# Kernel tuning notes

Hardware: AMD Instinct MI355X
Metric: run time of the kernel (lower is better)

The kernel has to match this reference:

```python
import jax, jax.numpy as jnp
import numpy as np

E, D, H, B = 8, 64, 512, 32768  # n_experts, state_dim, hidden width, batch
IN = D + 3  # x, t, sin(omega*t), cos(omega*t)


def setup_inputs() -> dict:
    key = jax.random.key(0)
    ks = jax.random.split(key, 12)
    s = 0.02
    return {
        "t": jax.random.uniform(ks[0], (1,), dtype=jnp.float32),
        "x": jax.random.normal(ks[1], (B, D), dtype=jnp.float32),
        "expert_weights": jax.random.uniform(ks[2], (B, E), dtype=jnp.float32),
        "omega": jnp.arange(1, E + 1, dtype=jnp.float32),  # omega_i = i+1
        "W1": jax.random.normal(ks[3], (E, H, IN), dtype=jnp.float32) * s,
        "b1": jnp.zeros((E, H), dtype=jnp.float32),
        "W2": jax.random.normal(ks[4], (E, H, H), dtype=jnp.float32) * s,
        "b2": jnp.zeros((E, H), dtype=jnp.float32),
        "W3": jax.random.normal(ks[5], (E, H, H), dtype=jnp.float32) * s,
        "b3": jnp.zeros((E, H), dtype=jnp.float32),
        "W4": jax.random.normal(ks[6], (E, D, H), dtype=jnp.float32) * s,
        "b4": jnp.zeros((E, D), dtype=jnp.float32),
    }


def reference(t, x, expert_weights, omega, W1, b1, W2, b2, W3, b3, W4, b4):
    # Dense path of ExpertODEEnsemble.forward: all experts active.
    nB = x.shape[0]
    tb = jnp.broadcast_to(t, (nB,))                       # (B,)
    wt = omega[:, None] * tb[None, :]                     # (E, B)
    # Per-expert inputs: [x, t, sin(wt), cos(wt)] -> (E, B, D+3)
    xe = jnp.broadcast_to(x[None], (E, nB, D))
    te = jnp.broadcast_to(tb[None, :, None], (E, nB, 1))
    inp = jnp.concatenate([xe, te, jnp.sin(wt)[..., None], jnp.cos(wt)[..., None]], axis=-1)
    h = jnp.tanh(jnp.einsum('ebi,ehi->ebh', inp, W1) + b1[:, None, :])
    h = jnp.tanh(jnp.einsum('ebh,egh->ebg', h, W2) + b2[:, None, :])
    h = jnp.tanh(jnp.einsum('ebh,egh->ebg', h, W3) + b3[:, None, :])
    dyn = jnp.einsum('ebh,edh->ebd', h, W4) + b4[:, None, :]   # (E, B, D)
    # Weighted combine: sum_e w[b,e] * dyn[e,b,:]
    dx_dt = jnp.einsum('be,ebd->bd', expert_weights, dyn)
    return dx_dt
```

## Files before the change

### kernel.cpp

```cpp
#include <hip/hip_runtime.h>
#include <hip/hip_bf16.h>


typedef unsigned short ushort_t;
typedef unsigned int u32;
typedef unsigned long long u64;
typedef __attribute__((ext_vector_type(8))) short short8;
typedef __attribute__((ext_vector_type(4))) float floatx4;
typedef __attribute__((ext_vector_type(16))) float floatx16;
typedef __attribute__((ext_vector_type(4))) int intx4;

#define W1A_OFF 0u
#define W2A_OFF 524288u
#define W3A_OFF 4718592u
#define W4A_OFF 8912896u
#define XB_OFF  9437184u
#define B1E_OFF 13631488u

#define SLOTB 16384
#define X_OFF_L 131072
#define SYNC_OFF 147456
#define SMEM_SZ 147552

static __device__ __forceinline__ u32 pk2bf(float a, float b) {
  union { __hip_bfloat162 h; u32 u; } v;
  v.h = __float22bfloat162_rn(make_float2(a, b));
  return v.u;
}

static __device__ __forceinline__ float pade_tanh(float x) {
  float x2 = x * x;
  float num = __builtin_fmaf(x2, __builtin_fmaf(x2, 1.0f, 105.0f), 945.0f);
  float den = __builtin_fmaf(x2, __builtin_fmaf(x2, 15.0f, 420.0f), 945.0f);
  return x * num * __builtin_amdgcn_rcpf(den);
}

static __device__ __forceinline__ void ald16(const void* g, void* l) {
  __builtin_amdgcn_global_load_lds((__attribute__((address_space(1))) void*)g,
                                   (__attribute__((address_space(3))) void*)l,
                                   16, 0, 0);
}

static __device__ __forceinline__ floatx16 mfma32(short8 a, short8 b, floatx16 c) {
  return __builtin_amdgcn_mfma_f32_32x32x16_bf16(a, b, c, 0, 0, 0);
}

static __device__ __forceinline__ int slot8(int g, int b) {
  return ((g + b) & 7) * SLOTB;
}

static __device__ __forceinline__ void waitge(const int* p, int tgt) {
  while (*(volatile const int*)p < tgt) __builtin_amdgcn_s_sleep(1);
  __asm__ __volatile__("" ::: "memory");
}

static __device__ __forceinline__ void waitge4(const int* p, int tgt) {
  for (;;) {
    __asm__ __volatile__("" ::: "memory");
    intx4 v = *(const intx4*)p;
    if (v[0] >= tgt && v[1] >= tgt && v[2] >= tgt && v[3] >= tgt) break;
    __builtin_amdgcn_s_sleep(1);
  }
  __asm__ __volatile__("" ::: "memory");
}

static __device__ __forceinline__ void guard_grp(const int* grp, int w, int base) {
  int tg0 = base + ((0 - w - 1) & 7) + 1;
  int tg1 = base + ((1 - w - 1) & 7) + 1;
  int tg2 = base + ((2 - w - 1) & 7) + 1;
  int tg3 = base + ((3 - w - 1) & 7) + 1;
  int tg4 = base + ((4 - w - 1) & 7) + 1;
  int tg5 = base + ((5 - w - 1) & 7) + 1;
  int tg6 = base + ((6 - w - 1) & 7) + 1;
  int tg7 = base + ((7 - w - 1) & 7) + 1;
  for (;;) {
    __asm__ __volatile__("" ::: "memory");
    intx4 a = *(const intx4*)grp;
    intx4 b = *(const intx4*)(grp + 4);
    if (a[0] >= tg0 && a[1] >= tg1 && a[2] >= tg2 && a[3] >= tg3 &&
        b[0] >= tg4 && b[1] >= tg5 && b[2] >= tg6 && b[3] >= tg7) break;
    __builtin_amdgcn_s_sleep(1);
  }
  __asm__ __volatile__("" ::: "memory");
}

static __device__ __forceinline__ void bump(int* p, int lane) {
  __asm__ __volatile__("s_waitcnt lgkmcnt(0)" ::: "memory");
  if (lane == 0) atomicAdd(p, 1);
}

static __device__ __forceinline__ void bump_sig(int* p, int lane) {
  __builtin_amdgcn_sched_barrier(0);
  if (lane == 0) atomicAdd(p, 1);
}

__global__ __launch_bounds__(256) void prep_kernel(
    const float* __restrict__ t, const float* __restrict__ x,
    const float* __restrict__ omega, const float* __restrict__ W1,
    const float* __restrict__ b1, const float* __restrict__ W2,
    const float* __restrict__ W3, const float* __restrict__ W4,
    char* __restrict__ ws) {
  int i = blockIdx.x * 256 + threadIdx.x;
  if (i < 32768) {
    int e = i >> 12, d = i & 4095;
    int lane = d & 63, q = d >> 6;
    int ol = q & 1, kc = (q >> 1) & 3, w = q >> 3;
    int outr = w * 64 + ol * 32 + (lane & 31);
    int kg = kc * 2 + (lane >> 5);
    const float* s = W1 + (e * 512 + outr) * 67 + kg * 8;
    ((intx4*)(ws + W1A_OFF))[i] = (intx4){
        (int)pk2bf(s[0], s[1]), (int)pk2bf(s[2], s[3]),
        (int)pk2bf(s[4], s[5]), (int)pk2bf(s[6], s[7])};
    return;
  }
  i -= 32768;
  if (i < 262144) {
    int e = i >> 15, d = i & 32767;
    int lane = d & 63, q = d >> 6;
    int ol = q & 1, kc = (q >> 1) & 31, w = q >> 6;
    int outr = w * 64 + ol * 32 + (lane & 31);
    int kg = kc * 2 + (lane >> 5);
    const floatx4* s = (const floatx4*)(W2 + ((e << 9) + outr) * 512 + (kg << 3));
    floatx4 lo = s[0], hi = s[1];
    ((intx4*)(ws + W2A_OFF))[i] = (intx4){
        (int)pk2bf(lo[0], lo[1]), (int)pk2bf(lo[2], lo[3]),
        (int)pk2bf(hi[0], hi[1]), (int)pk2bf(hi[2], hi[3])};
    return;
  }
  i -= 262144;
  if (i < 262144) {
    int e = i >> 15, d = i & 32767;
    int lane = d & 63, q = d >> 6;
    int ol = q & 1, kc = (q >> 1) & 31, w = q >> 6;
    int outr = w * 64 + ol * 32 + (lane & 31);
    int kg = kc * 2 + (lane >> 5);
    const floatx4* s = (const floatx4*)(W3 + ((e << 9) + outr) * 512 + (kg << 3));
    floatx4 lo = s[0], hi = s[1];
    ((intx4*)(ws + W3A_OFF))[i] = (intx4){
        (int)pk2bf(lo[0], lo[1]), (int)pk2bf(lo[2], lo[3]),
        (int)pk2bf(hi[0], hi[1]), (int)pk2bf(hi[2], hi[3])};
    return;
  }
  i -= 262144;
  if (i < 32768) {
    int e = i >> 12, d = i & 4095;
    int lane = d & 63, q = d >> 6;
    int kc = q & 31, o4 = q >> 5;
    int outr = o4 * 32 + (lane & 31);
    int kg = kc * 2 + (lane >> 5);
    const floatx4* s = (const floatx4*)(W4 + ((e << 6) + outr) * 512 + (kg << 3));
    floatx4 lo = s[0], hi = s[1];
    ((intx4*)(ws + W4A_OFF))[i] = (intx4){
        (int)pk2bf(lo[0], lo[1]), (int)pk2bf(lo[2], lo[3]),
        (int)pk2bf(hi[0], hi[1]), (int)pk2bf(hi[2], hi[3])};
    return;
  }
  i -= 32768;
  if (i < 262144) {
    const floatx4* s = (const floatx4*)(x + i * 8);
    floatx4 lo = s[0], hi = s[1];
    ((intx4*)(ws + XB_OFF))[i] = (intx4){
        (int)pk2bf(lo[0], lo[1]), (int)pk2bf(lo[2], lo[3]),
        (int)pk2bf(hi[0], hi[1]), (int)pk2bf(hi[2], hi[3])};
    return;
  }
  i -= 262144;
  if (i < 4096) {
    float tv = t[0];
    int e = i >> 9;
    float om = omega[e];
    ((float*)(ws + B1E_OFF))[i] = b1[i] + tv * W1[i * 67 + 64]
        + sinf(om * tv) * W1[i * 67 + 65] + cosf(om * tv) * W1[i * 67 + 66];
  }
}


static __device__ __forceinline__ void epi_write(
    floatx16 acc[2][4], char* __restrict__ act, int wbyte, int r31, int q1) {
#pragma unroll
  for (int ol = 0; ol < 2; ++ol) {
#pragma unroll
    for (int g = 0; g < 4; ++g) {
      int ko = ol * 4 + g;
      char* base = act + wbyte + (ko >> 1) * 4096
                   + (((ko & 1) * 32 + r31) << 4) + q1 * 8;
#pragma unroll
      for (int nt = 0; nt < 4; ++nt) {
        float v0 = pade_tanh(acc[ol][nt][4 * g + 0]);
        float v1 = pade_tanh(acc[ol][nt][4 * g + 1]);
        float v2 = pade_tanh(acc[ol][nt][4 * g + 2]);
        float v3 = pade_tanh(acc[ol][nt][4 * g + 3]);
        u32 lo = pk2bf(v0, v1), hi = pk2bf(v2, v3);
        *(u64*)(base + nt * 1024) = ((u64)hi << 32) | lo;
      }
    }
  }
}

static __device__ __forceinline__ void mlp_l1(
    char* __restrict__ act, const char* __restrict__ xreg,
    int* pub, int* l4c, int lane, int w, int q1, int r31,
    const char* __restrict__ Abase, const float* __restrict__ bias,
    int wbyte, int iter) {
  const int voff = lane * 16;
  const char* ap = Abase + w * 8192 + voff;

  floatx16 acc[2][4];
#pragma unroll
  for (int ol = 0; ol < 2; ++ol) {
    int fe0 = w * 64 + ol * 32 + 4 * q1;
#pragma unroll
    for (int g = 0; g < 4; ++g) {
      floatx4 bv = *(const floatx4*)(bias + fe0 + 8 * g);
#pragma unroll
      for (int nt = 0; nt < 4; ++nt) {
        acc[ol][nt][4 * g + 0] = bv[0];
        acc[ol][nt][4 * g + 1] = bv[1];
        acc[ol][nt][4 * g + 2] = bv[2];
        acc[ol][nt][4 * g + 3] = bv[3];
      }
    }
  }
  const char* xb0 = xreg + voff;
  short8 b0 = *(const short8*)(xb0);
  short8 b1v = *(const short8*)(xb0 + 1024);
  short8 b2 = *(const short8*)(xb0 + 2048);
  short8 b3 = *(const short8*)(xb0 + 3072);
  short8 a0 = *(const short8*)(ap);
  short8 a1 = *(const short8*)(ap + 1024);

#pragma unroll
  for (int j = 0; j < 4; ++j) {
    int jn = (j < 3) ? (j + 1) : 3;
    const char* xn = xreg + jn * 4096 + voff;
    const char* apn = (j < 3) ? (ap + 2048) : ap;
    short8 an0 = *(const short8*)(apn);
    short8 an1 = *(const short8*)(apn + 1024);
    short8 bn0 = *(const short8*)(xn);
    short8 bn1 = *(const short8*)(xn + 1024);
    short8 bn2 = *(const short8*)(xn + 2048);
    short8 bn3 = *(const short8*)(xn + 3072);
    __builtin_amdgcn_s_setprio(1);
    acc[0][0] = mfma32(a0, b0, acc[0][0]);
    acc[0][1] = mfma32(a0, b1v, acc[0][1]);
    acc[0][2] = mfma32(a0, b2, acc[0][2]);
    acc[0][3] = mfma32(a0, b3, acc[0][3]);
    acc[1][0] = mfma32(a1, b0, acc[1][0]);
    acc[1][1] = mfma32(a1, b1v, acc[1][1]);
    acc[1][2] = mfma32(a1, b2, acc[1][2]);
    acc[1][3] = mfma32(a1, b3, acc[1][3]);
    __builtin_amdgcn_s_setprio(0);
    a0 = an0; a1 = an1;
    b0 = bn0; b1v = bn1; b2 = bn2; b3 = bn3;
    ap = apn;
  }
  if (iter > 0) waitge4(l4c + ((((w + 1) & 7) >> 2) << 2), iter);
  epi_write(acc, act, wbyte, r31, q1);
  bump(pub + w, lane);
}

static __device__ __forceinline__ void mlp_mid(
    char* __restrict__ act, int* pub, int* grp, int lane, int w, int q1, int r31,
    const char* __restrict__ Abase, const float* __restrict__ bias,
    int pub_tgt, int rbase, int wbyte, int gbase) {
  const int voff = lane * 16;
  const char* spA = Abase + w * 65536 + voff;

  floatx16 acc[2][4];
#pragma unroll
  for (int ol = 0; ol < 2; ++ol) {
    int fe0 = w * 64 + ol * 32 + 4 * q1;
#pragma unroll
    for (int g = 0; g < 4; ++g) {
      floatx4 bv = *(const floatx4*)(bias + fe0 + 8 * g);
#pragma unroll
      for (int nt = 0; nt < 4; ++nt) {
        acc[ol][nt][4 * g + 0] = bv[0];
        acc[ol][nt][4 * g + 1] = bv[1];
        acc[ol][nt][4 * g + 2] = bv[2];
        acc[ol][nt][4 * g + 3] = bv[3];
      }
    }
  }
  const char* gb = act + slot8(w, rbase) + voff;
  const char* ap = spA + (4 * w) * 2048;
  short8 b0 = *(const short8*)(gb);
  short8 b1v = *(const short8*)(gb + 1024);
  short8 b2 = *(const short8*)(gb + 2048);
  short8 b3 = *(const short8*)(gb + 3072);
  short8 a0 = *(const short8*)(ap);
  short8 a1 = *(const short8*)(ap + 1024);

#pragma unroll 1
  for (int i = 0; i < 8; ++i) {
#pragma unroll
    for (int j = 0; j < 4; ++j) {
      const char* apn;
      const char* gbn = gb;
      const char* bsl;
      if (j < 3) {
        apn = ap + 2048;
        bsl = gb + (j + 1) * 4096;
      } else if (i < 7) {
        int g2 = (w - i - 1) & 7;
        waitge(pub + g2, pub_tgt);
        gbn = act + slot8(g2, rbase) + voff;
        apn = spA + (4 * g2) * 2048;
        bsl = gbn;
      } else {
        apn = ap; bsl = gb;
      }
      short8 an0 = *(const short8*)(apn);
      short8 an1 = *(const short8*)(apn + 1024);
      short8 bn0 = *(const short8*)(bsl);
      short8 bn1 = *(const short8*)(bsl + 1024);
      short8 bn2 = *(const short8*)(bsl + 2048);
      short8 bn3 = *(const short8*)(bsl + 3072);
      __builtin_amdgcn_s_setprio(1);
      acc[0][0] = mfma32(a0, b0, acc[0][0]);
      acc[0][1] = mfma32(a0, b1v, acc[0][1]);
      acc[0][2] = mfma32(a0, b2, acc[0][2]);
      acc[0][3] = mfma32(a0, b3, acc[0][3]);
      acc[1][0] = mfma32(a1, b0, acc[1][0]);
      acc[1][1] = mfma32(a1, b1v, acc[1][1]);
      acc[1][2] = mfma32(a1, b2, acc[1][2]);
      acc[1][3] = mfma32(a1, b3, acc[1][3]);
      __builtin_amdgcn_s_setprio(0);
      a0 = an0; a1 = an1;
      b0 = bn0; b1v = bn1; b2 = bn2; b3 = bn3;
      ap = apn; gb = gbn;
    }
    bump_sig(grp + w, lane);
  }

  guard_grp(grp, w, gbase);
  epi_write(acc, act, wbyte, r31, q1);
  bump(pub + w, lane);
}

extern "C" __global__ __launch_bounds__(512) void fused_kernel(
    const char* __restrict__ ws, const float* __restrict__ b2,
    const float* __restrict__ b3, const float* __restrict__ b4,
    const float* __restrict__ ew, float* __restrict__ out) {
  extern __shared__ char smem[];
  char* act = smem;
  char* xreg = smem + X_OFF_L;
  int* l4c = (int*)(smem + SYNC_OFF);
  int* pub = l4c + 8;
  int* grp = l4c + 16;

  const int t = threadIdx.x, lane = t & 63, w = t >> 6;
  const int q1 = lane >> 5, r31 = lane & 31;
  const int row0 = blockIdx.x << 7;
  const int voff = lane * 16;

  if (t < 24) ((int*)(smem + SYNC_OFF))[t] = 0;

  const ushort_t* xb = (const ushort_t*)(ws + XB_OFF);
#pragma unroll
  for (int s = 0; s < 2; ++s) {
    int u = w + 8 * s, v = u >> 2, nt = u & 3;
    ald16(xb + (row0 + nt * 32 + r31) * 64 + (2 * v + q1) * 8,
          xreg + v * 4096 + nt * 1024);
  }
  __syncthreads();

  for (int i = (7 - w) * 7; i > 0; --i) __builtin_amdgcn_s_sleep(1);

  const int rt = w & 3, kh = w >> 2;
  const int row_l4 = row0 + rt * 32 + r31;
  const int e0 = blockIdx.x & 7;
  floatx16 oacc[2] = {};

  for (int it = 0; it < 8; ++it) {
    const int e = (e0 + it) & 7;
    int b1s = (3 * it + 1) & 7;
    int b2s = (3 * it + 2) & 7;
    int b3s = (3 * it + 3) & 7;

    mlp_l1(act, xreg, pub, l4c, lane, w, q1, r31,
           (const char*)ws + W1A_OFF + e * 65536,
           (const float*)(ws + B1E_OFF) + e * 512, slot8(w, b1s), it);
    mlp_mid(act, pub, grp, lane, w, q1, r31,
            (const char*)ws + W2A_OFF + e * 524288, b2 + e * 512,
            3 * it + 1, b1s, slot8(w, b2s), 16 * it);
    mlp_mid(act, pub, grp, lane, w, q1, r31,
            (const char*)ws + W3A_OFF + e * 524288, b3 + e * 512,
            3 * it + 2, b2s, slot8(w, b3s), 16 * it + 8);

    {
      const char* spA4 = (const char*)ws + W4A_OFF + e * 65536 + voff;
      const float sc = ew[row_l4 * 8 + e];
      floatx16 acc4[2] = {};
      int g = 4 * kh + 3;
      waitge(pub + g, 3 * it + 3);
      const char* agb = spA4 + (4 * g) * 1024;
      const char* gb = act + slot8(g, b3s) + rt * 1024 + voff;
      short8 a0 = *(const short8*)(agb);
      short8 a1 = *(const short8*)(agb + 32768);
      short8 b = *(const short8*)(gb);
#pragma unroll 1
      for (int gl = 0; gl < 4; ++gl) {
#pragma unroll
        for (int j = 0; j < 4; ++j) {
          const char* agn = agb;
          const char* gbn = gb;
          const char* asl; const char* bsl;
          if (j < 3) {
            asl = agb + (j + 1) * 1024;
            bsl = gb + (j + 1) * 4096;
          } else if (gl < 3) {
            int g2 = g - 1;
            waitge(pub + g2, 3 * it + 3);
            agn = spA4 + (4 * g2) * 1024;
            gbn = act + slot8(g2, b3s) + rt * 1024 + voff;
            asl = agn; bsl = gbn;
          } else {
            asl = agb; bsl = gb;
          }
          short8 an0 = *(const short8*)(asl);
          short8 an1 = *(const short8*)(asl + 32768);
          short8 bn = *(const short8*)(bsl);
          __builtin_amdgcn_s_setprio(1);
          acc4[0] = mfma32(a0, b, acc4[0]);
          acc4[1] = mfma32(a1, b, acc4[1]);
          __builtin_amdgcn_s_setprio(0);
          a0 = an0; a1 = an1; b = bn;
          agb = agn; gb = gbn;
        }
        g = g - 1;
      }
      bump_sig(l4c + w, lane);
      if (kh == 0) {
        const float* bp = b4 + e * 64;
#pragma unroll
        for (int ol = 0; ol < 2; ++ol) {
          int fe0 = ol * 32 + 4 * q1;
#pragma unroll
          for (int g2 = 0; g2 < 4; ++g2) {
            floatx4 bv = *(const floatx4*)(bp + fe0 + 8 * g2);
            oacc[ol][4 * g2 + 0] += sc * (acc4[ol][4 * g2 + 0] + bv[0]);
            oacc[ol][4 * g2 + 1] += sc * (acc4[ol][4 * g2 + 1] + bv[1]);
            oacc[ol][4 * g2 + 2] += sc * (acc4[ol][4 * g2 + 2] + bv[2]);
            oacc[ol][4 * g2 + 3] += sc * (acc4[ol][4 * g2 + 3] + bv[3]);
          }
        }
      } else {
#pragma unroll
        for (int ol = 0; ol < 2; ++ol)
#pragma unroll
          for (int i = 0; i < 16; ++i) oacc[ol][i] += sc * acc4[ol][i];
      }
    }
  }

  __syncthreads();
  if (kh == 1) {
#pragma unroll
    for (int ol = 0; ol < 2; ++ol)
#pragma unroll
      for (int g = 0; g < 4; ++g) {
        floatx4 p = {oacc[ol][4 * g + 0], oacc[ol][4 * g + 1],
                     oacc[ol][4 * g + 2], oacc[ol][4 * g + 3]};
        *(floatx4*)(act + rt * 8192 + ol * 4096 + g * 1024 + lane * 16) = p;
      }
  }
  __syncthreads();
  if (kh == 0) {
    float* orow = out + (size_t)row_l4 * 64;
#pragma unroll
    for (int ol = 0; ol < 2; ++ol)
#pragma unroll
      for (int g = 0; g < 4; ++g) {
        floatx4 p = *(const floatx4*)(act + rt * 8192 + ol * 4096 + g * 1024 + lane * 16);
        floatx4 v = {oacc[ol][4 * g + 0] + p[0], oacc[ol][4 * g + 1] + p[1],
                     oacc[ol][4 * g + 2] + p[2], oacc[ol][4 * g + 3] + p[3]};
        *(floatx4*)(orow + ol * 32 + 8 * g + 4 * q1) = v;
      }
  }
}

extern "C" void kernel_launch(void* const* d_in, const int* in_sizes, int n_in,
                              void* d_out, int out_size, void* d_ws, size_t ws_size,
                              hipStream_t stream) {
  const float* t  = (const float*)d_in[0];
  const float* x  = (const float*)d_in[1];
  const float* ew = (const float*)d_in[2];
  const float* om = (const float*)d_in[3];
  const float* W1 = (const float*)d_in[4];
  const float* b1 = (const float*)d_in[5];
  const float* W2 = (const float*)d_in[6];
  const float* b2 = (const float*)d_in[7];
  const float* W3 = (const float*)d_in[8];
  const float* b3 = (const float*)d_in[9];
  const float* W4 = (const float*)d_in[10];
  const float* b4 = (const float*)d_in[11];
  char* ws = (char*)d_ws;
  float* out = (float*)d_out;
  (void)in_sizes; (void)n_in; (void)ws_size; (void)out_size;

  static int smem_set = 0;
  if (!smem_set) {
    hipFuncSetAttribute((const void*)fused_kernel,
                        hipFuncAttributeMaxDynamicSharedMemorySize, SMEM_SZ);
    smem_set = 1;
  }
  prep_kernel<<<3344, 256, 0, stream>>>(t, x, om, W1, b1, W2, W3, W4, ws);
  fused_kernel<<<256, 512, SMEM_SZ, stream>>>(ws, b2, b3, b4, ew, out);
}
```

Measured before the change: 420.9 us.

## Pin experts to XCDs with per-expert partial outputs and separate reduce kernel

Adds a new main path. Each block reads its XCD id and takes a ticket from a per-XCD atomic counter, so it handles one expert (the XCD id) over 1024 rows, instead of every block looping over all experts for 128 rows. This keeps each expert's weights resident in one XCD's L2. Each block writes weighted per-expert partials to a large workspace buffer, and a separate reduce kernel sums the 8 experts into the output. The cost is an extra 64 MB of partial writes and reads plus one more launch. The old kernel is kept as a fallback when the workspace is too small.

```diff
diff --git a/kernel.cpp b/kernel.cpp
--- a/kernel.cpp
+++ b/kernel.cpp
@@ -16,11 +16,16 @@
 #define W4A_OFF 8912896u
 #define XB_OFF  9437184u
 #define B1E_OFF 13631488u
+#define TICK_OFF 13647872u
+#define PART_OFF 13648128u
+#define WS_NEED  80756992u
 
 #define SLOTB 16384
+#define SYNC2_OFF 131072
+#define SMEM2_SZ 131200
 #define X_OFF_L 131072
-#define SYNC_OFF 147456
-#define SMEM_SZ 147552
+#define SYNCF_OFF 147456
+#define SMEMF_SZ 147552
 
 static __device__ __forceinline__ u32 pk2bf(float a, float b) {
   union { __hip_bfloat162 h; u32 u; } v;
@@ -88,7 +93,6 @@
   __asm__ __volatile__("s_waitcnt lgkmcnt(0)" ::: "memory");
   if (lane == 0) atomicAdd(p, 1);
 }
-
 static __device__ __forceinline__ void bump_sig(int* p, int lane) {
   __builtin_amdgcn_sched_barrier(0);
   if (lane == 0) atomicAdd(p, 1);
@@ -99,7 +103,7 @@
     const float* __restrict__ omega, const float* __restrict__ W1,
     const float* __restrict__ b1, const float* __restrict__ W2,
     const float* __restrict__ W3, const float* __restrict__ W4,
-    char* __restrict__ ws) {
+    char* __restrict__ ws, int big) {
   int i = blockIdx.x * 256 + threadIdx.x;
   if (i < 32768) {
     int e = i >> 12, d = i & 4095;
@@ -171,9 +175,11 @@
     float om = omega[e];
     ((float*)(ws + B1E_OFF))[i] = b1[i] + tv * W1[i * 67 + 64]
         + sinf(om * tv) * W1[i * 67 + 65] + cosf(om * tv) * W1[i * 67 + 66];
-  }
-}
-
+    return;
+  }
+  i -= 4096;
+  if (i < 8 && big) ((int*)(ws + TICK_OFF))[i] = 0;
+}
 
 static __device__ __forceinline__ void epi_write(
     floatx16 acc[2][4], char* __restrict__ act, int wbyte, int r31, int q1) {
@@ -197,14 +203,252 @@
   }
 }
 
-static __device__ __forceinline__ void mlp_l1(
+static __device__ __forceinline__ void mlp_mid(
+    char* __restrict__ act, int* pub, int* grp, int lane, int w, int q1, int r31,
+    const char* __restrict__ Abase, const float* __restrict__ bias,
+    int pub_tgt, int rbase, int wbyte, int gbase) {
+  const int voff = lane * 16;
+  const char* spA = Abase + w * 65536 + voff;
+
+  floatx16 acc[2][4];
+#pragma unroll
+  for (int ol = 0; ol < 2; ++ol) {
+    int fe0 = w * 64 + ol * 32 + 4 * q1;
+#pragma unroll
+    for (int g = 0; g < 4; ++g) {
+      floatx4 bv = *(const floatx4*)(bias + fe0 + 8 * g);
+#pragma unroll
+      for (int nt = 0; nt < 4; ++nt) {
+        acc[ol][nt][4 * g + 0] = bv[0];
+        acc[ol][nt][4 * g + 1] = bv[1];
+        acc[ol][nt][4 * g + 2] = bv[2];
+        acc[ol][nt][4 * g + 3] = bv[3];
+      }
+    }
+  }
+  const char* gb = act + slot8(w, rbase) + voff;
+  const char* ap = spA + (4 * w) * 2048;
+  short8 b0 = *(const short8*)(gb);
+  short8 b1v = *(const short8*)(gb + 1024);
+  short8 b2 = *(const short8*)(gb + 2048);
+  short8 b3 = *(const short8*)(gb + 3072);
+  short8 a0 = *(const short8*)(ap);
+  short8 a1 = *(const short8*)(ap + 1024);
+
+#pragma unroll 1
+  for (int i = 0; i < 8; ++i) {
+#pragma unroll
+    for (int j = 0; j < 4; ++j) {
+      const char* apn;
+      const char* gbn = gb;
+      const char* bsl;
+      if (j < 3) {
+        apn = ap + 2048;
+        bsl = gb + (j + 1) * 4096;
+      } else if (i < 7) {
+        int g2 = (w - i - 1) & 7;
+        waitge(pub + g2, pub_tgt);
+        gbn = act + slot8(g2, rbase) + voff;
+        apn = spA + (4 * g2) * 2048;
+        bsl = gbn;
+      } else {
+        apn = ap; bsl = gb;
+      }
+      short8 an0 = *(const short8*)(apn);
+      short8 an1 = *(const short8*)(apn + 1024);
+      short8 bn0 = *(const short8*)(bsl);
+      short8 bn1 = *(const short8*)(bsl + 1024);
+      short8 bn2 = *(const short8*)(bsl + 2048);
+      short8 bn3 = *(const short8*)(bsl + 3072);
+      __builtin_amdgcn_s_setprio(1);
+      acc[0][0] = mfma32(a0, b0, acc[0][0]);
+      acc[0][1] = mfma32(a0, b1v, acc[0][1]);
+      acc[0][2] = mfma32(a0, b2, acc[0][2]);
+      acc[0][3] = mfma32(a0, b3, acc[0][3]);
+      acc[1][0] = mfma32(a1, b0, acc[1][0]);
+      acc[1][1] = mfma32(a1, b1v, acc[1][1]);
+      acc[1][2] = mfma32(a1, b2, acc[1][2]);
+      acc[1][3] = mfma32(a1, b3, acc[1][3]);
+      __builtin_amdgcn_s_setprio(0);
+      a0 = an0; a1 = an1;
+      b0 = bn0; b1v = bn1; b2 = bn2; b3 = bn3;
+      ap = apn; gb = gbn;
+    }
+    bump_sig(grp + w, lane);
+  }
+  guard_grp(grp, w, gbase);
+  epi_write(acc, act, wbyte, r31, q1);
+  bump(pub + w, lane);
+}
+
+static __device__ __forceinline__ void mlp_l1_glob(
+    char* __restrict__ act, int* pub, int* l4c, int lane, int w, int q1, int r31,
+    const char* __restrict__ Abase, const float* __restrict__ bias,
+    const char* __restrict__ xl, int wbyte, int it) {
+  const int voff = lane * 16;
+  const char* ap = Abase + w * 8192 + voff;
+
+  floatx16 acc[2][4];
+#pragma unroll
+  for (int ol = 0; ol < 2; ++ol) {
+    int fe0 = w * 64 + ol * 32 + 4 * q1;
+#pragma unroll
+    for (int g = 0; g < 4; ++g) {
+      floatx4 bv = *(const floatx4*)(bias + fe0 + 8 * g);
+#pragma unroll
+      for (int nt = 0; nt < 4; ++nt) {
+        acc[ol][nt][4 * g + 0] = bv[0];
+        acc[ol][nt][4 * g + 1] = bv[1];
+        acc[ol][nt][4 * g + 2] = bv[2];
+        acc[ol][nt][4 * g + 3] = bv[3];
+      }
+    }
+  }
+  short8 b0 = *(const short8*)(xl);
+  short8 b1v = *(const short8*)(xl + 4096);
+  short8 b2 = *(const short8*)(xl + 8192);
+  short8 b3 = *(const short8*)(xl + 12288);
+  short8 a0 = *(const short8*)(ap);
+  short8 a1 = *(const short8*)(ap + 1024);
+
+#pragma unroll
+  for (int j = 0; j < 4; ++j) {
+    int kcn = (j < 3) ? (j + 1) : 3;
+    const char* xn = xl + kcn * 32;
+    const char* apn = (j < 3) ? (ap + 2048) : ap;
+    short8 an0 = *(const short8*)(apn);
+    short8 an1 = *(const short8*)(apn + 1024);
+    short8 bn0 = *(const short8*)(xn);
+    short8 bn1 = *(const short8*)(xn + 4096);
+    short8 bn2 = *(const short8*)(xn + 8192);
+    short8 bn3 = *(const short8*)(xn + 12288);
+    __builtin_amdgcn_s_setprio(1);
+    acc[0][0] = mfma32(a0, b0, acc[0][0]);
+    acc[0][1] = mfma32(a0, b1v, acc[0][1]);
+    acc[0][2] = mfma32(a0, b2, acc[0][2]);
+    acc[0][3] = mfma32(a0, b3, acc[0][3]);
+    acc[1][0] = mfma32(a1, b0, acc[1][0]);
+    acc[1][1] = mfma32(a1, b1v, acc[1][1]);
+    acc[1][2] = mfma32(a1, b2, acc[1][2]);
+    acc[1][3] = mfma32(a1, b3, acc[1][3]);
+    __builtin_amdgcn_s_setprio(0);
+    a0 = an0; a1 = an1;
+    b0 = bn0; b1v = bn1; b2 = bn2; b3 = bn3;
+    ap = apn;
+  }
+  if (it > 0) { waitge4(l4c, it); waitge4(l4c + 4, it); }
+  epi_write(acc, act, wbyte, r31, q1);
+  bump(pub + w, lane);
+}
+
+extern "C" __global__ __launch_bounds__(512) void fused_kernel(
+    char* __restrict__ ws, const float* __restrict__ b2,
+    const float* __restrict__ b3, const float* __restrict__ b4,
+    const float* __restrict__ ew, float* __restrict__ out) {
+  extern __shared__ char smem[];
+  char* act = smem;
+  int* l4c = (int*)(smem + SYNC2_OFF);
+  int* pub = l4c + 8;
+  int* grp = l4c + 16;
+  (void)out;
+
+  const int t = threadIdx.x, lane = t & 63, w = t >> 6;
+  const int q1 = lane >> 5, r31 = lane & 31;
+  const int voff = lane * 16;
+
+  u32 xcd;
+  __asm__ __volatile__("s_getreg_b32 %0, hwreg(HW_REG_XCC_ID)" : "=s"(xcd));
+  xcd &= 7;
+
+  if (t < 24) ((int*)(smem + SYNC2_OFF))[t] = 0;
+  if (t == 0) {
+    int tk = atomicAdd((int*)(ws + TICK_OFF) + xcd, 1);
+    ((int*)(smem + SYNC2_OFF))[24] = tk;
+    ((int*)(smem + SYNC2_OFF))[25] = (int)xcd;
+  }
+  __syncthreads();
+  const int rg = ((int*)(smem + SYNC2_OFF))[24];
+  const int e  = ((int*)(smem + SYNC2_OFF))[25];
+
+  for (int i = (7 - w) * 7; i > 0; --i) __builtin_amdgcn_s_sleep(1);
+
+  const int o4 = w & 1, rt4 = w >> 1;
+  float* part = (float*)(ws + PART_OFF);
+
+  for (int it = 0; it < 8; ++it) {
+    const int row0 = rg * 1024 + it * 128;
+    int b1s = (3 * it + 1) & 7;
+    int b2s = (3 * it + 2) & 7;
+    int b3s = (3 * it + 3) & 7;
+    const char* xl = (const char*)ws + XB_OFF + (size_t)row0 * 128
+                     + r31 * 128 + q1 * 16;
+
+    mlp_l1_glob(act, pub, l4c, lane, w, q1, r31,
+                (const char*)ws + W1A_OFF + e * 65536,
+                (const float*)(ws + B1E_OFF) + e * 512, xl, slot8(w, b1s), it);
+    mlp_mid(act, pub, grp, lane, w, q1, r31,
+            (const char*)ws + W2A_OFF + e * 524288, b2 + e * 512,
+            3 * it + 1, b1s, slot8(w, b2s), 16 * it);
+    mlp_mid(act, pub, grp, lane, w, q1, r31,
+            (const char*)ws + W3A_OFF + e * 524288, b3 + e * 512,
+            3 * it + 2, b2s, slot8(w, b3s), 16 * it + 8);
+
+    {
+      const char* spA4 = (const char*)ws + W4A_OFF + e * 65536
+                         + o4 * 32768 + voff;
+      const int row_l4 = row0 + rt4 * 32 + r31;
+      floatx16 acc4 = {};
+#pragma unroll 1
+      for (int g = 0; g < 8; ++g) {
+        waitge(pub + g, 3 * it + 3);
+        const char* gb = act + slot8(g, b3s) + rt4 * 1024 + voff;
+        const char* apg = spA4 + g * 4096;
+#pragma unroll
+        for (int s = 0; s < 4; ++s) {
+          short8 a = *(const short8*)(apg + s * 1024);
+          short8 b = *(const short8*)(gb + s * 4096);
+          __builtin_amdgcn_s_setprio(1);
+          acc4 = mfma32(a, b, acc4);
+          __builtin_amdgcn_s_setprio(0);
+        }
+      }
+      bump_sig(l4c + w, lane);
+
+      const float sc = ew[row_l4 * 8 + e];
+      const float* bp = b4 + e * 64 + o4 * 32;
+      float* pr = part + ((size_t)e << 21) + (size_t)row_l4 * 64 + o4 * 32;
+#pragma unroll
+      for (int g2 = 0; g2 < 4; ++g2) {
+        floatx4 bv = *(const floatx4*)(bp + 8 * g2 + 4 * q1);
+        floatx4 v = {sc * (acc4[4 * g2 + 0] + bv[0]),
+                     sc * (acc4[4 * g2 + 1] + bv[1]),
+                     sc * (acc4[4 * g2 + 2] + bv[2]),
+                     sc * (acc4[4 * g2 + 3] + bv[3])};
+        *(floatx4*)(pr + 8 * g2 + 4 * q1) = v;
+      }
+    }
+  }
+}
+
+extern "C" __global__ __launch_bounds__(256) void reduce_kernel(
+    const float* __restrict__ part, float* __restrict__ out) {
+  size_t i = ((size_t)blockIdx.x * 256 + threadIdx.x) * 4;
+  floatx4 a = *(const floatx4*)(part + i);
+#pragma unroll
+  for (int e = 1; e < 8; ++e) {
+    floatx4 p = *(const floatx4*)(part + ((size_t)e << 21) + i);
+    a[0] += p[0]; a[1] += p[1]; a[2] += p[2]; a[3] += p[3];
+  }
+  *(floatx4*)(out + i) = a;
+}
+
+static __device__ __forceinline__ void mlp_l1_lds(
     char* __restrict__ act, const char* __restrict__ xreg,
     int* pub, int* l4c, int lane, int w, int q1, int r31,
     const char* __restrict__ Abase, const float* __restrict__ bias,
     int wbyte, int iter) {
   const int voff = lane * 16;
   const char* ap = Abase + w * 8192 + voff;
-
   floatx16 acc[2][4];
 #pragma unroll
   for (int ol = 0; ol < 2; ++ol) {
@@ -228,7 +472,6 @@
   short8 b3 = *(const short8*)(xb0 + 3072);
   short8 a0 = *(const short8*)(ap);
   short8 a1 = *(const short8*)(ap + 1024);
-
 #pragma unroll
   for (int j = 0; j < 4; ++j) {
     int jn = (j < 3) ? (j + 1) : 3;
@@ -259,93 +502,14 @@
   bump(pub + w, lane);
 }
 
-static __device__ __forceinline__ void mlp_mid(
-    char* __restrict__ act, int* pub, int* grp, int lane, int w, int q1, int r31,
-    const char* __restrict__ Abase, const float* __restrict__ bias,
-    int pub_tgt, int rbase, int wbyte, int gbase) {
-  const int voff = lane * 16;
-  const char* spA = Abase + w * 65536 + voff;
-
-  floatx16 acc[2][4];
-#pragma unroll
-  for (int ol = 0; ol < 2; ++ol) {
-    int fe0 = w * 64 + ol * 32 + 4 * q1;
-#pragma unroll
-    for (int g = 0; g < 4; ++g) {
-      floatx4 bv = *(const floatx4*)(bias + fe0 + 8 * g);
-#pragma unroll
-      for (int nt = 0; nt < 4; ++nt) {
-        acc[ol][nt][4 * g + 0] = bv[0];
-        acc[ol][nt][4 * g + 1] = bv[1];
-        acc[ol][nt][4 * g + 2] = bv[2];
-        acc[ol][nt][4 * g + 3] = bv[3];
-      }
-    }
-  }
-  const char* gb = act + slot8(w, rbase) + voff;
-  const char* ap = spA + (4 * w) * 2048;
-  short8 b0 = *(const short8*)(gb);
-  short8 b1v = *(const short8*)(gb + 1024);
-  short8 b2 = *(const short8*)(gb + 2048);
-  short8 b3 = *(const short8*)(gb + 3072);
-  short8 a0 = *(const short8*)(ap);
-  short8 a1 = *(const short8*)(ap + 1024);
-
-#pragma unroll 1
-  for (int i = 0; i < 8; ++i) {
-#pragma unroll
-    for (int j = 0; j < 4; ++j) {
-      const char* apn;
-      const char* gbn = gb;
-      const char* bsl;
-      if (j < 3) {
-        apn = ap + 2048;
-        bsl = gb + (j + 1) * 4096;
-      } else if (i < 7) {
-        int g2 = (w - i - 1) & 7;
-        waitge(pub + g2, pub_tgt);
-        gbn = act + slot8(g2, rbase) + voff;
-        apn = spA + (4 * g2) * 2048;
-        bsl = gbn;
-      } else {
-        apn = ap; bsl = gb;
-      }
-      short8 an0 = *(const short8*)(apn);
-      short8 an1 = *(const short8*)(apn + 1024);
-      short8 bn0 = *(const short8*)(bsl);
-      short8 bn1 = *(const short8*)(bsl + 1024);
-      short8 bn2 = *(const short8*)(bsl + 2048);
-      short8 bn3 = *(const short8*)(bsl + 3072);
-      __builtin_amdgcn_s_setprio(1);
-      acc[0][0] = mfma32(a0, b0, acc[0][0]);
-      acc[0][1] = mfma32(a0, b1v, acc[0][1]);
-      acc[0][2] = mfma32(a0, b2, acc[0][2]);
-      acc[0][3] = mfma32(a0, b3, acc[0][3]);
-      acc[1][0] = mfma32(a1, b0, acc[1][0]);
-      acc[1][1] = mfma32(a1, b1v, acc[1][1]);
-      acc[1][2] = mfma32(a1, b2, acc[1][2]);
-      acc[1][3] = mfma32(a1, b3, acc[1][3]);
-      __builtin_amdgcn_s_setprio(0);
-      a0 = an0; a1 = an1;
-      b0 = bn0; b1v = bn1; b2 = bn2; b3 = bn3;
-      ap = apn; gb = gbn;
-    }
-    bump_sig(grp + w, lane);
-  }
-
-  guard_grp(grp, w, gbase);
-  epi_write(acc, act, wbyte, r31, q1);
-  bump(pub + w, lane);
-}
-
-extern "C" __global__ __launch_bounds__(512) void fused_kernel(
+extern "C" __global__ __launch_bounds__(512) void fused_fb(
     const char* __restrict__ ws, const float* __restrict__ b2,
     const float* __restrict__ b3, const float* __restrict__ b4,
     const float* __restrict__ ew, float* __restrict__ out) {
   extern __shared__ char smem[];
   char* act = smem;
   char* xreg = smem + X_OFF_L;
-  int* l4c = (int*)(smem + SYNC_OFF);
+  int* l4c = (int*)(smem + SYNCF_OFF);
   int* pub = l4c + 8;
   int* grp = l4c + 16;
 
@@ -354,8 +518,7 @@
   const int row0 = blockIdx.x << 7;
   const int voff = lane * 16;
 
-  if (t < 24) ((int*)(smem + SYNC_OFF))[t] = 0;
-
+  if (t < 24) ((int*)(smem + SYNCF_OFF))[t] = 0;
   const ushort_t* xb = (const ushort_t*)(ws + XB_OFF);
 #pragma unroll
   for (int s = 0; s < 2; ++s) {
@@ -364,7 +527,6 @@
           xreg + v * 4096 + nt * 1024);
   }
   __syncthreads();
-
   for (int i = (7 - w) * 7; i > 0; --i) __builtin_amdgcn_s_sleep(1);
 
   const int rt = w & 3, kh = w >> 2;
@@ -377,17 +539,15 @@
     int b1s = (3 * it + 1) & 7;
     int b2s = (3 * it + 2) & 7;
     int b3s = (3 * it + 3) & 7;
-
-    mlp_l1(act, xreg, pub, l4c, lane, w, q1, r31,
-           (const char*)ws + W1A_OFF + e * 65536,
-           (const float*)(ws + B1E_OFF) + e * 512, slot8(w, b1s), it);
+    mlp_l1_lds(act, xreg, pub, l4c, lane, w, q1, r31,
+               (const char*)ws + W1A_OFF + e * 65536,
+               (const float*)(ws + B1E_OFF) + e * 512, slot8(w, b1s), it);
     mlp_mid(act, pub, grp, lane, w, q1, r31,
             (const char*)ws + W2A_OFF + e * 524288, b2 + e * 512,
             3 * it + 1, b1s, slot8(w, b2s), 16 * it);
     mlp_mid(act, pub, grp, lane, w, q1, r31,
             (const char*)ws + W3A_OFF + e * 524288, b3 + e * 512,
             3 * it + 2, b2s, slot8(w, b3s), 16 * it + 8);
-
     {
       const char* spA4 = (const char*)ws + W4A_OFF + e * 65536 + voff;
       const float sc = ew[row_l4 * 8 + e];
@@ -453,7 +613,6 @@
       }
     }
   }
-
   __syncthreads();
   if (kh == 1) {
 #pragma unroll
@@ -497,14 +656,22 @@
   const float* b4 = (const float*)d_in[11];
   char* ws = (char*)d_ws;
   float* out = (float*)d_out;
-  (void)in_sizes; (void)n_in; (void)ws_size; (void)out_size;
+  (void)in_sizes; (void)n_in; (void)out_size;
 
   static int smem_set = 0;
   if (!smem_set) {
     hipFuncSetAttribute((const void*)fused_kernel,
-                        hipFuncAttributeMaxDynamicSharedMemorySize, SMEM_SZ);
+                        hipFuncAttributeMaxDynamicSharedMemorySize, SMEM2_SZ);
+    hipFuncSetAttribute((const void*)fused_fb,
+                        hipFuncAttributeMaxDynamicSharedMemorySize, SMEMF_SZ);
     smem_set = 1;
   }
-  prep_kernel<<<3344, 256, 0, stream>>>(t, x, om, W1, b1, W2, W3, W4, ws);
-  fused_kernel<<<256, 512, SMEM_SZ, stream>>>(ws, b2, b3, b4, ew, out);
-}
+  int big = (ws_size >= (size_t)WS_NEED) ? 1 : 0;
+  prep_kernel<<<3345, 256, 0, stream>>>(t, x, om, W1, b1, W2, W3, W4, ws, big);
+  if (big) {
+    fused_kernel<<<256, 512, SMEM2_SZ, stream>>>(ws, b2, b3, b4, ew, out);
+    reduce_kernel<<<2048, 256, 0, stream>>>((const float*)(ws + PART_OFF), out);
+  } else {
+    fused_fb<<<256, 512, SMEMF_SZ, stream>>>(ws, b2, b3, b4, ew, out);
+  }
+}
```

Result: slower. 476.7 us (+13.3%).
